# Optimization experiments

Measured on AMD Instinct MI355X. Metric: run time of the kernel, lower is better.

The kernel has to match this reference:

```python
import jax, jax.numpy as jnp
import numpy as np

D = 2048
H = 16
HD = D // H
DFF = 8192
EPS = 1e-6


def rmsnorm(x, w):
    xf = x.astype(jnp.float32)
    var = jnp.mean(xf * xf, axis=-1, keepdims=True)
    return w * (xf * jax.lax.rsqrt(var + EPS)).astype(x.dtype)


def setup_inputs() -> dict:
    key = jax.random.key(0)
    ks = jax.random.split(key, 10)
    s = 0.02
    return {
        "hidden_states": jax.random.normal(ks[0], (2, 2048, D), jnp.float32),
        "wq": jax.random.normal(ks[1], (D, D), jnp.float32) * s,
        "wk": jax.random.normal(ks[2], (D, D), jnp.float32) * s,
        "wv": jax.random.normal(ks[3], (D, D), jnp.float32) * s,
        "wo": jax.random.normal(ks[4], (D, D), jnp.float32) * s,
        "w_gate": jax.random.normal(ks[5], (DFF, D), jnp.float32) * s,
        "w_up": jax.random.normal(ks[6], (DFF, D), jnp.float32) * s,
        "w_down": jax.random.normal(ks[7], (D, DFF), jnp.float32) * s,
        "ln1_w": jnp.ones((D,), jnp.float32),
        "ln2_w": jnp.ones((D,), jnp.float32),
    }


def reference(hidden_states, wq, wk, wv, wo, w_gate, w_up, w_down, ln1_w, ln2_w):
    B, S, _ = hidden_states.shape
    residual = hidden_states
    x = rmsnorm(hidden_states, ln1_w)
    # projections (torch Linear: y = x @ W.T), split heads -> [B,H,S,HD]
    q = (x @ wq.T).reshape(B, S, H, HD).transpose(0, 2, 1, 3)
    k = (x @ wk.T).reshape(B, S, H, HD).transpose(0, 2, 1, 3)
    v = (x @ wv.T).reshape(B, S, H, HD).transpose(0, 2, 1, 3)
    scores = jnp.einsum("bhqd,bhkd->bhqk", q, k) / np.sqrt(HD).astype(np.float32)
    causal = jnp.triu(jnp.ones((S, S), bool), k=1)  # True above diagonal -> masked
    scores = jnp.where(causal, -jnp.inf, scores)
    attn = jax.nn.softmax(scores, axis=-1)
    out = jnp.einsum("bhqk,bhkd->bhqd", attn, v)
    out = out.transpose(0, 2, 1, 3).reshape(B, S, D)
    out = out @ wo.T
    hidden = residual + out
    residual = hidden
    y = rmsnorm(hidden, ln2_w)
    gate = y @ w_gate.T
    up = y @ w_up.T
    mlp = (jax.nn.silu(gate) * up) @ w_down.T
    return residual + mlp
```

## Files before the change

kernel.cpp:

```cpp
#include <hip/hip_runtime.h>
#include <stdint.h>

#define D_MODEL 2048
#define NHEADS  16
#define HEADDIM 128
#define DFF     8192
#define BATCH   2
#define SEQ     2048
#define NTOK    (BATCH*SEQ)
#define EPS     1e-6f
#define QKV_RS  (3*D_MODEL)

typedef unsigned short u16;
typedef short  s16x8 __attribute__((ext_vector_type(8)));
typedef float  f32x4 __attribute__((ext_vector_type(4)));

__device__ __forceinline__ u16 f2bf(float f) {
  union { float f; uint32_t u; } v; v.f = f;
  uint32_t u = v.u;
  return (u16)((u + 0x7fffu + ((u >> 16) & 1u)) >> 16);
}
__device__ __forceinline__ float bf2f(u16 h) {
  union { uint32_t u; float f; } v; v.u = ((uint32_t)h) << 16;
  return v.f;
}

__device__ __forceinline__ void gload_lds16(const void* g, void* l) {
  __builtin_amdgcn_global_load_lds(
      (const __attribute__((address_space(1))) void*)g,
      (__attribute__((address_space(3))) void*)l, 16, 0, 0);
}

__device__ __forceinline__ f32x4 mfma16(s16x8 a, s16x8 b, f32x4 c) {
  return __builtin_amdgcn_mfma_f32_16x16x32_bf16(a, b, c, 0, 0, 0);
}

#define BAR()   asm volatile("s_barrier" ::: "memory")
#define LGK0()  asm volatile("s_waitcnt lgkmcnt(0)" ::: "memory")

__device__ __forceinline__ void cvt_one(const float* in, u16* out, int i) {
  float4 v = ((const float4*)in)[i];
  uint32_t lo = (uint32_t)f2bf(v.x) | ((uint32_t)f2bf(v.y) << 16);
  uint32_t hi = (uint32_t)f2bf(v.z) | ((uint32_t)f2bf(v.w) << 16);
  uint2 st; st.x = lo; st.y = hi;
  ((uint2*)out)[i] = st;
}

__global__ __launch_bounds__(256)
void cvt_kernel(const float* __restrict__ in, u16* __restrict__ out, int n4)
{
  int idx = blockIdx.x * 256 + threadIdx.x;
  int stride = gridDim.x * 256;
  for (int i = idx; i < n4; i += stride) cvt_one(in, out, i);
}

__global__ __launch_bounds__(256)
void cvt4_kernel(const float* __restrict__ a, const float* __restrict__ b,
                 const float* __restrict__ c, const float* __restrict__ d,
                 u16* __restrict__ oa, u16* __restrict__ ob,
                 u16* __restrict__ oc, u16* __restrict__ od, int n4)
{
  int idx = blockIdx.x * 256 + threadIdx.x;
  int stride = gridDim.x * 256;
  for (int i = idx; i < 4 * n4; i += stride) {
    int w = i / n4, j = i - w * n4;
    const float* s = (w == 0) ? a : (w == 1) ? b : (w == 2) ? c : d;
    u16* o = (w == 0) ? oa : (w == 1) ? ob : (w == 2) ? oc : od;
    cvt_one(s, o, j);
  }
}

__global__ __launch_bounds__(256)
void cvt2_kernel(const float* __restrict__ a, const float* __restrict__ b,
                 u16* __restrict__ oa, u16* __restrict__ ob, int n4)
{
  int idx = blockIdx.x * 256 + threadIdx.x;
  int stride = gridDim.x * 256;
  for (int i = idx; i < 2 * n4; i += stride) {
    int w = i / n4, j = i - w * n4;
    cvt_one(w ? b : a, w ? ob : oa, j);
  }
}

__global__ __launch_bounds__(256)
void rmsnorm_kernel(const float* __restrict__ x, const float* __restrict__ w,
                    u16* __restrict__ out)
{
  int row = blockIdx.x;
  int tid = threadIdx.x;
  const float4* xr = (const float4*)(x + (size_t)row * D_MODEL);
  float4 a = xr[tid];
  float4 b = xr[tid + 256];
  float ss = a.x*a.x + a.y*a.y + a.z*a.z + a.w*a.w
           + b.x*b.x + b.y*b.y + b.z*b.z + b.w*b.w;
#pragma unroll
  for (int o = 32; o > 0; o >>= 1) ss += __shfl_xor(ss, o);
  __shared__ float red[4];
  if ((tid & 63) == 0) red[tid >> 6] = ss;
  __syncthreads();
  float tot = red[0] + red[1] + red[2] + red[3];
  float sc = rsqrtf(tot * (1.0f / D_MODEL) + EPS);
  const float4* wr = (const float4*)w;
  float4 wa = wr[tid], wb = wr[tid + 256];
  u16* orow = out + (size_t)row * D_MODEL;
  uint2 s0, s1;
  s0.x = (uint32_t)f2bf(a.x*wa.x*sc) | ((uint32_t)f2bf(a.y*wa.y*sc) << 16);
  s0.y = (uint32_t)f2bf(a.z*wa.z*sc) | ((uint32_t)f2bf(a.w*wa.w*sc) << 16);
  s1.x = (uint32_t)f2bf(b.x*wb.x*sc) | ((uint32_t)f2bf(b.y*wb.y*sc) << 16);
  s1.y = (uint32_t)f2bf(b.z*wb.z*sc) | ((uint32_t)f2bf(b.w*wb.w*sc) << 16);
  ((uint2*)orow)[tid] = s0;
  ((uint2*)orow)[tid + 256] = s1;
}

#define BM 128
#define BN 128
#define BK 64

template<int EPI>
__global__ __launch_bounds__(256, 2)
void gemm_bt(const u16* __restrict__ A, const u16* __restrict__ B,
             void* __restrict__ Cout, const float* __restrict__ aux,
             int M, int N, int K)
{
  __shared__ u16 As[BM * BK];
  __shared__ u16 Bs[BN * BK];
  const int nbn = N / BN;
  int bid = blockIdx.x;
  int swz = (gridDim.x & 7) ? bid : ((bid & 7) * (gridDim.x >> 3) + (bid >> 3));
  const int bm = swz / nbn, bn = swz % nbn;
  const int m0 = bm * BM, n0 = bn * BN;
  const int tid = threadIdx.x;
  const int lane = tid & 63;
  const int wm = tid >> 7, wn = (tid >> 6) & 1;
  const int lr = lane & 15, lg = lane >> 4;

  f32x4 acc[4][4] = {};

  for (int k0 = 0; k0 < K; k0 += BK) {
#pragma unroll
    for (int i = 0; i < 4; ++i) {
      int c = i * 256 + tid;
      int row = c >> 3, cr = c & 7;
      int g = cr ^ (row & 7);
      gload_lds16(A + (size_t)(m0 + row) * K + k0 + (g << 3), &As[c * 8]);
      gload_lds16(B + (size_t)(n0 + row) * K + k0 + (g << 3), &Bs[c * 8]);
    }
    __syncthreads();
#pragma unroll
    for (int kk = 0; kk < BK; kk += 32) {
      s16x8 a[4], b[4];
#pragma unroll
      for (int m = 0; m < 4; ++m) {
        int row = wm * 64 + m * 16 + lr;
        int j = (kk >> 3) + lg;
        a[m] = *(const s16x8*)&As[row * BK + ((j ^ (row & 7)) << 3)];
      }
#pragma unroll
      for (int n = 0; n < 4; ++n) {
        int row = wn * 64 + n * 16 + lr;
        int j = (kk >> 3) + lg;
        b[n] = *(const s16x8*)&Bs[row * BK + ((j ^ (row & 7)) << 3)];
      }
#pragma unroll
      for (int m = 0; m < 4; ++m)
#pragma unroll
        for (int n = 0; n < 4; ++n)
          acc[m][n] = mfma16(a[m], b[n], acc[m][n]);
    }
    __syncthreads();
  }

#pragma unroll
  for (int m = 0; m < 4; ++m) {
#pragma unroll
    for (int n = 0; n < 4; ++n) {
      int col = n0 + wn * 64 + n * 16 + lr;
#pragma unroll
      for (int r = 0; r < 4; ++r) {
        int row = m0 + wm * 64 + m * 16 + lg * 4 + r;
        size_t idx = (size_t)row * N + col;
        float v = acc[m][n][r];
        if (EPI == 0) {
          ((u16*)Cout)[idx] = f2bf(v);
        } else if (EPI == 1) {
          float up = bf2f(((u16*)Cout)[idx]);
          float s = v / (1.0f + __expf(-v));
          ((u16*)Cout)[idx] = f2bf(s * up);
        } else if (EPI == 2) {
          ((float*)Cout)[idx] = aux[idx] + v;
        } else {
          ((float*)Cout)[idx] += v;
        }
      }
    }
  }
}

template<int EPI>
__global__ __launch_bounds__(512, 2)
void gemm256(const u16* __restrict__ A, const u16* __restrict__ B,
             void* __restrict__ Cout, const float* __restrict__ aux,
             int M, int N, int K)
{
  __shared__ u16 As[2][2][256 * 32];
  __shared__ u16 Bs[2][2][256 * 32];
  const int nbn = N >> 8;
  const int bm = blockIdx.x / nbn, bn = blockIdx.x % nbn;
  const int m0 = bm << 8, n0 = bn << 8;
  const int tid = threadIdx.x, lane = tid & 63;
  const int wid = tid >> 6;
  const int wm = wid >> 2, wn = wid & 3;
  const int lr = lane & 15, lg = lane >> 4;

  f32x4 acc[8][4] = {};

  auto stA = [&](int td, int ts, int kh) {
    const u16* src = A + (size_t)m0 * K + ts * 64 + kh * 32;
    u16* dst = &As[td & 1][kh][0];
#pragma unroll
    for (int i = 0; i < 2; ++i) {
      int c = i * 512 + tid;
      int row = c >> 2, sl = c & 3;
      int g = sl ^ ((row >> 1) & 3);
      gload_lds16(src + (size_t)row * K + (g << 3), dst + (c << 3));
    }
  };
  auto stB = [&](int td, int ts, int kh) {
    const u16* src = B + (size_t)n0 * K + ts * 64 + kh * 32;
    u16* dst = &Bs[td & 1][kh][0];
#pragma unroll
    for (int i = 0; i < 2; ++i) {
      int c = i * 512 + tid;
      int row = c >> 2, sl = c & 3;
      int g = sl ^ ((row >> 1) & 3);
      gload_lds16(src + (size_t)row * K + (g << 3), dst + (c << 3));
    }
  };
  auto rdA = [&](int t, int kh, int m) -> s16x8 {
    int row = wm * 128 + m * 16 + lr;
    int sl = lg ^ ((row >> 1) & 3);
    return *(const s16x8*)&As[t & 1][kh][row * 32 + (sl << 3)];
  };
  auto rdB = [&](int t, int kh, int n) -> s16x8 {
    int row = wn * 64 + n * 16 + lr;
    int sl = lg ^ ((row >> 1) & 3);
    return *(const s16x8*)&Bs[t & 1][kh][row * 32 + (sl << 3)];
  };

  const int nt = K >> 6;

  stA(0, 0, 0); stB(0, 0, 0);
  stA(0, 0, 1); stB(0, 0, 1);
  asm volatile("s_waitcnt vmcnt(4)" ::: "memory");
  BAR();

  s16x8 aA[4], aB[4], bA[4], bB[4];
#pragma unroll
  for (int n = 0; n < 4; ++n) bA[n] = rdB(0, 0, n);
#pragma unroll
  for (int m = 0; m < 4; ++m) aA[m] = rdA(0, 0, m);
  stA(1, 1, 0); stB(1, 1, 0);
  asm volatile("s_waitcnt vmcnt(4)" ::: "memory");
  BAR();

#pragma unroll 1
  for (int t = 0; t < nt; ++t) {
    const int tp1 = t + 1, tp2 = t + 2;
    const int s1 = tp1 < nt ? tp1 : nt - 1;
    const int s2 = tp2 < nt ? tp2 : nt - 1;

    stA(tp1, s1, 1);
#pragma unroll
    for (int m = 0; m < 4; ++m) aB[m] = rdA(t, 0, m + 4);
    __builtin_amdgcn_s_setprio(1);
#pragma unroll
    for (int m = 0; m < 4; ++m)
#pragma unroll
      for (int n = 0; n < 4; ++n) acc[m][n] = mfma16(aA[m], bA[n], acc[m][n]);
    __builtin_amdgcn_s_setprio(0);

    stB(tp1, s1, 1);
#pragma unroll
    for (int n = 0; n < 4; ++n) bB[n] = rdB(t, 1, n);
#pragma unroll
    for (int m = 0; m < 4; ++m) aA[m] = rdA(t, 1, m);
    __builtin_amdgcn_s_setprio(1);
#pragma unroll
    for (int m = 0; m < 4; ++m)
#pragma unroll
      for (int n = 0; n < 4; ++n) acc[m + 4][n] = mfma16(aB[m], bA[n], acc[m + 4][n]);
    __builtin_amdgcn_s_setprio(0);
    asm volatile("s_waitcnt vmcnt(4)" ::: "memory");
    BAR();

    stA(tp2, s2, 0);
#pragma unroll
    for (int m = 0; m < 4; ++m) aB[m] = rdA(t, 1, m + 4);
    __builtin_amdgcn_s_setprio(1);
#pragma unroll
    for (int m = 0; m < 4; ++m)
#pragma unroll
      for (int n = 0; n < 4; ++n) acc[m][n] = mfma16(aA[m], bB[n], acc[m][n]);
    __builtin_amdgcn_s_setprio(0);

    stB(tp2, s2, 0);
#pragma unroll
    for (int n = 0; n < 4; ++n) bA[n] = rdB(tp1, 0, n);
#pragma unroll
    for (int m = 0; m < 4; ++m) aA[m] = rdA(tp1, 0, m);
    __builtin_amdgcn_s_setprio(1);
#pragma unroll
    for (int m = 0; m < 4; ++m)
#pragma unroll
      for (int n = 0; n < 4; ++n) acc[m + 4][n] = mfma16(aB[m], bB[n], acc[m + 4][n]);
    __builtin_amdgcn_s_setprio(0);
    asm volatile("s_waitcnt vmcnt(4)" ::: "memory");
    BAR();
  }

  asm volatile("s_waitcnt vmcnt(0)" ::: "memory");

#pragma unroll
  for (int m = 0; m < 8; ++m) {
#pragma unroll
    for (int n = 0; n < 4; ++n) {
      int col = n0 + wn * 64 + n * 16 + lr;
#pragma unroll
      for (int r = 0; r < 4; ++r) {
        int row = m0 + wm * 128 + m * 16 + lg * 4 + r;
        size_t idx = (size_t)row * N + col;
        float v = acc[m][n][r];
        if (EPI == 0) {
          ((u16*)Cout)[idx] = f2bf(v);
        } else if (EPI == 1) {
          float up = bf2f(((u16*)Cout)[idx]);
          float s = v / (1.0f + __expf(-v));
          ((u16*)Cout)[idx] = f2bf(s * up);
        } else if (EPI == 2) {
          ((float*)Cout)[idx] = aux[idx] + v;
        } else {
          ((float*)Cout)[idx] += v;
        }
      }
    }
  }
}

#define QBLK 128
#define KVBLK 64

__global__ __launch_bounds__(256, 2)
void attn_kernel(const u16* __restrict__ QKV, u16* __restrict__ O)
{
  __shared__ u16 Ks[2][KVBLK * HEADDIM];
  __shared__ u16 Vt[HEADDIM * KVBLK];
  __shared__ u16 Pw[4][32 * KVBLK];

  const int bid = blockIdx.x;
  const int p  = bid & 15;
  const int h  = (bid >> 4) & (NHEADS - 1);
  const int b  = bid >> 8;
  const int tid = threadIdx.x, lane = tid & 63, wid = tid >> 6;
  const int lr = lane & 15, lg = lane >> 4;
  const size_t tokbase = (size_t)b * SEQ;
  const int hoff = h * HEADDIM;
  const int qrow0 = p * 64 + wid * 16;
  const int qrow1 = (31 - p) * 64 + wid * 16;
  const int nkb = 32 - p;
  const float scale = 0.08838834764831845f;

  s16x8 qf[2][4];
#pragma unroll
  for (int c = 0; c < 4; ++c) {
    qf[0][c] = *(const s16x8*)(QKV + (tokbase + qrow0 + lr) * QKV_RS
                               + hoff + c * 32 + lg * 8);
    qf[1][c] = *(const s16x8*)(QKV + (tokbase + qrow1 + lr) * QKV_RS
                               + hoff + c * 32 + lg * 8);
  }

  f32x4 o_acc[2][8] = {};
  float m_run[2][4], l_run[2][4];
#pragma unroll
  for (int m = 0; m < 2; ++m)
#pragma unroll
    for (int r = 0; r < 4; ++r) { m_run[m][r] = -1e30f; l_run[m][r] = 0.0f; }

  s16x8 v0[2], v1[2];

  {
    const u16* kbase = QKV + tokbase * QKV_RS + D_MODEL + hoff;
#pragma unroll
    for (int it = 0; it < 4; ++it) {
      int c = it * 256 + tid;
      int row = c >> 4, cr = c & 15;
      int g = cr ^ (row & 7);
      gload_lds16(kbase + (size_t)row * QKV_RS + g * 8, &Ks[0][c * 8]);
    }
    const u16* vbase = QKV + tokbase * QKV_RS + 2 * D_MODEL + hoff;
#pragma unroll
    for (int i = 0; i < 2; ++i) {
      int pi = i * 256 + tid;
      int rp = pi >> 4, dc = pi & 15;
      const u16* vp = vbase + (size_t)(rp * 2) * QKV_RS + dc * 8;
      v0[i] = *(const s16x8*)vp;
      v1[i] = *(const s16x8*)(vp + QKV_RS);
    }
    uint32_t* vt = (uint32_t*)&Vt[0];
#pragma unroll
    for (int i = 0; i < 2; ++i) {
      int pi = i * 256 + tid;
      int rp = pi >> 4, dc = pi & 15;
      int k0 = rp * 2;
      int base = ((k0 >> 3) ^ (dc & 7)) * 4 + ((k0 >> 1) & 3);
#pragma unroll
      for (int j = 0; j < 8; ++j)
        vt[(dc * 8 + j) * (KVBLK / 2) + base] =
            (uint32_t)(u16)v0[i][j] | ((uint32_t)(u16)v1[i][j] << 16);
    }
  }
  __syncthreads();

  for (int kb = 0; kb < nkb; ++kb) {
    const int buf = kb & 1;
    const bool nb = (kb + 1 < nkb);
    const bool act0 = (kb <= p);

    if (nb) {
      const u16* kbase = QKV + (tokbase + (size_t)(kb + 1) * KVBLK) * QKV_RS + D_MODEL + hoff;
#pragma unroll
      for (int it = 0; it < 4; ++it) {
        int c = it * 256 + tid;
        int row = c >> 4, cr = c & 15;
        int g = cr ^ (row & 7);
        gload_lds16(kbase + (size_t)row * QKV_RS + g * 8, &Ks[buf ^ 1][c * 8]);
      }
      const u16* vbase = QKV + (tokbase + (size_t)(kb + 1) * KVBLK) * QKV_RS + 2 * D_MODEL + hoff;
#pragma unroll
      for (int i = 0; i < 2; ++i) {
        int pi = i * 256 + tid;
        int rp = pi >> 4, dc = pi & 15;
        const u16* vp = vbase + (size_t)(rp * 2) * QKV_RS + dc * 8;
        v0[i] = *(const s16x8*)vp;
        v1[i] = *(const s16x8*)(vp + QKV_RS);
      }
    }

    f32x4 s_acc[2][4] = {};
#pragma unroll
    for (int kk = 0; kk < 4; ++kk) {
      s16x8 kf[4];
#pragma unroll
      for (int n = 0; n < 4; ++n) {
        int row = n * 16 + lr;
        int ch = (kk * 4 + lg) ^ (row & 7);
        kf[n] = *(const s16x8*)&Ks[buf][row * HEADDIM + ch * 8];
      }
#pragma unroll
      for (int m = 0; m < 2; ++m) {
        if (m == 0 && !act0) continue;
#pragma unroll
        for (int n = 0; n < 4; ++n)
          s_acc[m][n] = mfma16(qf[m][kk], kf[n], s_acc[m][n]);
      }
    }

#pragma unroll
    for (int m = 0; m < 2; ++m) {
      if (m == 0 && !act0) continue;
      const int qb_ = (m == 0) ? qrow0 : qrow1;
      float tmax[4] = {-1e30f, -1e30f, -1e30f, -1e30f};
      float sv[4][4];
#pragma unroll
      for (int n = 0; n < 4; ++n) {
        int key = kb * KVBLK + n * 16 + lr;
#pragma unroll
        for (int r = 0; r < 4; ++r) {
          int q = qb_ + lg * 4 + r;
          float s = s_acc[m][n][r] * scale;
          if (key > q) s = -1e30f;
          sv[n][r] = s;
          tmax[r] = fmaxf(tmax[r], s);
        }
      }
#pragma unroll
      for (int o = 1; o < 16; o <<= 1)
#pragma unroll
        for (int r = 0; r < 4; ++r)
          tmax[r] = fmaxf(tmax[r], __shfl_xor(tmax[r], o));

      float pf[4], psum[4];
#pragma unroll
      for (int r = 0; r < 4; ++r) {
        float mn = fmaxf(m_run[m][r], tmax[r]);
        pf[r] = __expf(m_run[m][r] - mn);
        m_run[m][r] = mn;
        psum[r] = 0.0f;
      }
#pragma unroll
      for (int n = 0; n < 4; ++n) {
        int keyl = n * 16 + lr;
#pragma unroll
        for (int r = 0; r < 4; ++r) {
          float pv = __expf(sv[n][r] - m_run[m][r]);
          psum[r] += pv;
          int ql = m * 16 + lg * 4 + r;
          int ch = (keyl >> 3) ^ (ql & 7);
          Pw[wid][ql * KVBLK + ch * 8 + (keyl & 7)] = f2bf(pv);
        }
      }
#pragma unroll
      for (int o = 1; o < 16; o <<= 1)
#pragma unroll
        for (int r = 0; r < 4; ++r)
          psum[r] += __shfl_xor(psum[r], o);
#pragma unroll
      for (int r = 0; r < 4; ++r)
        l_run[m][r] = l_run[m][r] * pf[r] + psum[r];
#pragma unroll
      for (int t = 0; t < 8; ++t)
#pragma unroll
        for (int r = 0; r < 4; ++r)
          o_acc[m][t][r] *= pf[r];
    }

#pragma unroll
    for (int kk = 0; kk < 2; ++kk) {
      s16x8 pa[2];
#pragma unroll
      for (int m = 0; m < 2; ++m) {
        int ql = m * 16 + lr;
        int ch = (kk * 4 + lg) ^ (ql & 7);
        pa[m] = *(const s16x8*)&Pw[wid][ql * KVBLK + ch * 8];
      }
#pragma unroll
      for (int t = 0; t < 8; ++t) {
        int d = t * 16 + lr;
        int ch = (kk * 4 + lg) ^ ((d >> 3) & 7);
        s16x8 vf = *(const s16x8*)&Vt[d * KVBLK + ch * 8];
#pragma unroll
        for (int m = 0; m < 2; ++m) {
          if (m == 0 && !act0) continue;
          o_acc[m][t] = mfma16(pa[m], vf, o_acc[m][t]);
        }
      }
    }

    __syncthreads();
    if (nb) {
      uint32_t* vt = (uint32_t*)&Vt[0];
#pragma unroll
      for (int i = 0; i < 2; ++i) {
        int pi = i * 256 + tid;
        int rp = pi >> 4, dc = pi & 15;
        int k0 = rp * 2;
        int base = ((k0 >> 3) ^ (dc & 7)) * 4 + ((k0 >> 1) & 3);
#pragma unroll
        for (int j = 0; j < 8; ++j)
          vt[(dc * 8 + j) * (KVBLK / 2) + base] =
              (uint32_t)(u16)v0[i][j] | ((uint32_t)(u16)v1[i][j] << 16);
      }
    }
    __syncthreads();
  }

#pragma unroll
  for (int m = 0; m < 2; ++m)
#pragma unroll
    for (int t = 0; t < 8; ++t)
#pragma unroll
      for (int r = 0; r < 4; ++r) {
        int q = ((m == 0) ? qrow0 : qrow1) + lg * 4 + r;
        O[(tokbase + q) * D_MODEL + hoff + t * 16 + lr] =
            f2bf(o_acc[m][t][r] / l_run[m][r]);
      }
}

extern "C" void kernel_launch(void* const* d_in, const int* in_sizes, int n_in,
                              void* d_out, int out_size, void* d_ws, size_t ws_size,
                              hipStream_t stream)
{
  const float* hidden = (const float*)d_in[0];
  const float* wq    = (const float*)d_in[1];
  const float* wk    = (const float*)d_in[2];
  const float* wv    = (const float*)d_in[3];
  const float* wo    = (const float*)d_in[4];
  const float* wgate = (const float*)d_in[5];
  const float* wup   = (const float*)d_in[6];
  const float* wdown = (const float*)d_in[7];
  const float* ln1   = (const float*)d_in[8];
  const float* ln2   = (const float*)d_in[9];
  float* out = (float*)d_out;

  const size_t TD = (size_t)NTOK * D_MODEL;
  const size_t DD = (size_t)D_MODEL * D_MODEL;
  const size_t FD = (size_t)DFF * D_MODEL;

  u16* XN  = (u16*)d_ws;
  u16* QKV = XN + TD;
  u16* AO  = QKV + 3 * TD;
  u16* WB  = AO + TD;
  u16* GU  = WB + FD;

  dim3 b256(256), b512(512);

  cvt4_kernel<<<dim3(2048), b256, 0, stream>>>(
      wq, wk, wv, wo, WB + 0 * DD, WB + 1 * DD, WB + 2 * DD, WB + 3 * DD,
      (int)(DD / 4));

  rmsnorm_kernel<<<dim3(NTOK), b256, 0, stream>>>(hidden, ln1, XN);

  gemm256<0><<<dim3(16 * 24), b512, 0, stream>>>(XN, WB, QKV, nullptr, NTOK, 3 * D_MODEL, D_MODEL);

  attn_kernel<<<dim3(BATCH * NHEADS * (SEQ / QBLK)), b256, 0, stream>>>(QKV, AO);

  gemm_bt<2><<<dim3(32 * 16), b256, 0, stream>>>(AO, WB + 3 * DD, out, hidden, NTOK, D_MODEL, D_MODEL);

  cvt2_kernel<<<dim3(4096), b256, 0, stream>>>(wgate, wup, WB, QKV, (int)(FD / 4));

  rmsnorm_kernel<<<dim3(NTOK), b256, 0, stream>>>(out, ln2, XN);

  gemm256<0><<<dim3(16 * 32), b512, 0, stream>>>(XN, QKV, GU, nullptr, NTOK, DFF, D_MODEL);
  gemm256<1><<<dim3(16 * 32), b512, 0, stream>>>(XN, WB, GU, nullptr, NTOK, DFF, D_MODEL);

  cvt_kernel<<<dim3(8192), b256, 0, stream>>>(wdown, QKV, (int)(FD / 4));

  gemm_bt<3><<<dim3(32 * 16), b256, 0, stream>>>(GU, QKV, out, nullptr, NTOK, D_MODEL, DFF);
}
```

Baseline: 900.9 us.

## Restructure 256x256 GEMM mainloop into 8-phase ping-pong schedule with K=64 LDS tiles

Changes the LDS layout of the 256-tile GEMM to hold full 64-wide K slices per row half with an 8-way XOR swizzle, and replaces the 4-phase loop with an 8-phase schedule. Each phase interleaves one quarter-tile of global-to-LDS loads with LDS reads and a 4x2x2 MFMA quadrant. The aim is finer-grained overlap of loads with MFMA and fewer bank conflicts. It adds many more barriers and lgkmcnt(0) waits per iteration, which may stall the waves.

```diff
diff --git a/kernel.cpp b/kernel.cpp
--- a/kernel.cpp
+++ b/kernel.cpp
@@ -37,6 +37,7 @@
 
 #define BAR()   asm volatile("s_barrier" ::: "memory")
 #define LGK0()  asm volatile("s_waitcnt lgkmcnt(0)" ::: "memory")
+#define VMC6()  asm volatile("s_waitcnt vmcnt(6)" ::: "memory")
 
 __device__ __forceinline__ void cvt_one(const float* in, u16* out, int i) {
   float4 v = ((const float4*)in)[i];
@@ -202,8 +203,8 @@
              void* __restrict__ Cout, const float* __restrict__ aux,
              int M, int N, int K)
 {
-  __shared__ u16 As[2][2][256 * 32];
-  __shared__ u16 Bs[2][2][256 * 32];
+  __shared__ u16 As[2][2 * 8192];
+  __shared__ u16 Bs[2][2 * 8192];
   const int nbn = N >> 8;
   const int bm = blockIdx.x / nbn, bn = blockIdx.x % nbn;
   const int m0 = bm << 8, n0 = bn << 8;
@@ -213,109 +214,97 @@
   const int lr = lane & 15, lg = lane >> 4;
 
   f32x4 acc[8][4] = {};
-
-  auto stA = [&](int td, int ts, int kh) {
-    const u16* src = A + (size_t)m0 * K + ts * 64 + kh * 32;
-    u16* dst = &As[td & 1][kh][0];
+  s16x8 aE[8], aO[8], bE[4], bO[4];
+
+  auto stA = [&](int buf, int rh, int ts) {
+    const u16* src = A + (size_t)m0 * K + ts * 64;
+    u16* dst = &As[buf][rh * 8192];
 #pragma unroll
     for (int i = 0; i < 2; ++i) {
       int c = i * 512 + tid;
-      int row = c >> 2, sl = c & 3;
-      int g = sl ^ ((row >> 1) & 3);
-      gload_lds16(src + (size_t)row * K + (g << 3), dst + (c << 3));
+      int r = c >> 3, cr = c & 7;
+      int grow = ((r >> 6) << 7) | (rh << 6) | (r & 63);
+      int g = cr ^ (r & 7);
+      gload_lds16(src + (size_t)grow * K + (g << 3), dst + c * 8);
     }
   };
-  auto stB = [&](int td, int ts, int kh) {
-    const u16* src = B + (size_t)n0 * K + ts * 64 + kh * 32;
-    u16* dst = &Bs[td & 1][kh][0];
+  auto stB = [&](int buf, int rh, int ts) {
+    const u16* src = B + (size_t)n0 * K + ts * 64;
+    u16* dst = &Bs[buf][rh * 8192];
 #pragma unroll
     for (int i = 0; i < 2; ++i) {
       int c = i * 512 + tid;
-      int row = c >> 2, sl = c & 3;
-      int g = sl ^ ((row >> 1) & 3);
-      gload_lds16(src + (size_t)row * K + (g << 3), dst + (c << 3));
+      int r = c >> 3, cr = c & 7;
+      int grow = ((r >> 5) << 6) | (rh << 5) | (r & 31);
+      int g = cr ^ (r & 7);
+      gload_lds16(src + (size_t)grow * K + (g << 3), dst + c * 8);
     }
   };
-  auto rdA = [&](int t, int kh, int m) -> s16x8 {
-    int row = wm * 128 + m * 16 + lr;
-    int sl = lg ^ ((row >> 1) & 3);
-    return *(const s16x8*)&As[t & 1][kh][row * 32 + (sl << 3)];
+  auto rdA = [&](int buf, int mh, s16x8* d) {
+#pragma unroll
+    for (int i = 0; i < 4; ++i)
+#pragma unroll
+      for (int kk = 0; kk < 2; ++kk) {
+        int sr = wm * 64 + i * 16 + lr;
+        int jj = (kk * 4 + lg) ^ (sr & 7);
+        d[i * 2 + kk] = *(const s16x8*)&As[buf][mh * 8192 + sr * 64 + (jj << 3)];
+      }
   };
-  auto rdB = [&](int t, int kh, int n) -> s16x8 {
-    int row = wn * 64 + n * 16 + lr;
-    int sl = lg ^ ((row >> 1) & 3);
-    return *(const s16x8*)&Bs[t & 1][kh][row * 32 + (sl << 3)];
+  auto rdB = [&](int buf, int nh, s16x8* d) {
+#pragma unroll
+    for (int j = 0; j < 2; ++j)
+#pragma unroll
+      for (int kk = 0; kk < 2; ++kk) {
+        int sr = wn * 32 + j * 16 + lr;
+        int jj = (kk * 4 + lg) ^ (sr & 7);
+        d[j * 2 + kk] = *(const s16x8*)&Bs[buf][nh * 8192 + sr * 64 + (jj << 3)];
+      }
   };
+  auto MF = [&](int mh, int nh, const s16x8* a, const s16x8* b) {
+    __builtin_amdgcn_s_setprio(1);
+#pragma unroll
+    for (int i = 0; i < 4; ++i)
+#pragma unroll
+      for (int j = 0; j < 2; ++j)
+#pragma unroll
+        for (int kk = 0; kk < 2; ++kk)
+          acc[mh * 4 + i][nh * 2 + j] =
+              mfma16(a[i * 2 + kk], b[j * 2 + kk], acc[mh * 4 + i][nh * 2 + j]);
+    __builtin_amdgcn_s_setprio(0);
+  };
 
   const int nt = K >> 6;
 
-  stA(0, 0, 0); stB(0, 0, 0);
-  stA(0, 0, 1); stB(0, 0, 1);
-  asm volatile("s_waitcnt vmcnt(4)" ::: "memory");
+  stA(0, 0, 0); stB(0, 0, 0); stB(0, 1, 0); stA(0, 1, 0);
+  stA(1, 0, 1); stB(1, 0, 1); stB(1, 1, 1); stA(1, 1, 1);
+  VMC6();
   BAR();
-
-  s16x8 aA[4], aB[4], bA[4], bB[4];
-#pragma unroll
-  for (int n = 0; n < 4; ++n) bA[n] = rdB(0, 0, n);
-#pragma unroll
-  for (int m = 0; m < 4; ++m) aA[m] = rdA(0, 0, m);
-  stA(1, 1, 0); stB(1, 1, 0);
-  asm volatile("s_waitcnt vmcnt(4)" ::: "memory");
+  rdA(0, 0, aE);
+  LGK0();
   BAR();
 
 #pragma unroll 1
-  for (int t = 0; t < nt; ++t) {
-    const int tp1 = t + 1, tp2 = t + 2;
-    const int s1 = tp1 < nt ? tp1 : nt - 1;
-    const int s2 = tp2 < nt ? tp2 : nt - 1;
-
-    stA(tp1, s1, 1);
-#pragma unroll
-    for (int m = 0; m < 4; ++m) aB[m] = rdA(t, 0, m + 4);
-    __builtin_amdgcn_s_setprio(1);
-#pragma unroll
-    for (int m = 0; m < 4; ++m)
-#pragma unroll
-      for (int n = 0; n < 4; ++n) acc[m][n] = mfma16(aA[m], bA[n], acc[m][n]);
-    __builtin_amdgcn_s_setprio(0);
-
-    stB(tp1, s1, 1);
-#pragma unroll
-    for (int n = 0; n < 4; ++n) bB[n] = rdB(t, 1, n);
-#pragma unroll
-    for (int m = 0; m < 4; ++m) aA[m] = rdA(t, 1, m);
-    __builtin_amdgcn_s_setprio(1);
-#pragma unroll
-    for (int m = 0; m < 4; ++m)
-#pragma unroll
-      for (int n = 0; n < 4; ++n) acc[m + 4][n] = mfma16(aB[m], bA[n], acc[m + 4][n]);
-    __builtin_amdgcn_s_setprio(0);
-    asm volatile("s_waitcnt vmcnt(4)" ::: "memory");
-    BAR();
-
-    stA(tp2, s2, 0);
-#pragma unroll
-    for (int m = 0; m < 4; ++m) aB[m] = rdA(t, 1, m + 4);
-    __builtin_amdgcn_s_setprio(1);
-#pragma unroll
-    for (int m = 0; m < 4; ++m)
-#pragma unroll
-      for (int n = 0; n < 4; ++n) acc[m][n] = mfma16(aA[m], bB[n], acc[m][n]);
-    __builtin_amdgcn_s_setprio(0);
-
-    stB(tp2, s2, 0);
-#pragma unroll
-    for (int n = 0; n < 4; ++n) bA[n] = rdB(tp1, 0, n);
-#pragma unroll
-    for (int m = 0; m < 4; ++m) aA[m] = rdA(tp1, 0, m);
-    __builtin_amdgcn_s_setprio(1);
-#pragma unroll
-    for (int m = 0; m < 4; ++m)
-#pragma unroll
-      for (int n = 0; n < 4; ++n) acc[m + 4][n] = mfma16(aB[m], bB[n], acc[m + 4][n]);
-    __builtin_amdgcn_s_setprio(0);
-    asm volatile("s_waitcnt vmcnt(4)" ::: "memory");
-    BAR();
+  for (int it = 0; it < (nt >> 1); ++it) {
+    const int u = it << 1;
+    const int s2 = (u + 2 < nt) ? u + 2 : nt - 1;
+    const int s3 = (u + 3 < nt) ? u + 3 : nt - 1;
+
+    rdB(0, 0, bE); stA(0, 0, s2); BAR(); LGK0();
+    MF(0, 0, aE, bE); BAR();
+    rdB(0, 1, bO); stB(0, 0, s2); BAR(); LGK0();
+    MF(0, 1, aE, bO); BAR();
+    rdA(0, 1, aO); stB(0, 1, s2); BAR(); LGK0();
+    MF(1, 1, aO, bO); BAR();
+    rdA(1, 0, aE); stA(0, 1, s2); BAR(); LGK0();
+    MF(1, 0, aO, bE); VMC6(); BAR();
+    rdB(1, 0, bE); stA(1, 0, s3); BAR(); LGK0();
+    MF(0, 0, aE, bE); BAR();
+    rdB(1, 1, bO); stB(1, 0, s3); BAR(); LGK0();
+    MF(0, 1, aE, bO); BAR();
+    rdA(1, 1, aO); stB(1, 1, s3); BAR(); LGK0();
+    MF(1, 1, aO, bO); BAR();
+    rdA(0, 0, aE); stA(1, 1, s3); BAR(); LGK0();
+    MF(1, 0, aO, bE); VMC6(); BAR();
   }
 
   asm volatile("s_waitcnt vmcnt(0)" ::: "memory");
```

Measured after the change: 850.9 us. 5.5% less time.
